# Kernel tuning notes

Measured on AMD Instinct MI355X. Metric: run time of the kernel, lower is better.

The kernel has to match this reference:

```python
import jax, jax.numpy as jnp
import numpy as np

B, L, DIM = 2, 2048, 1024
H, D = 16, 64  # n_heads, head_dim; H*D == DIM


def setup_inputs() -> dict:
    key = jax.random.key(0)
    ks = jax.random.split(key, 5)
    s = 0.02
    return {
        "x": jax.random.normal(ks[0], (B, L, DIM), dtype=jnp.float32),
        "Wq": jax.random.normal(ks[1], (DIM, H * D), dtype=jnp.float32) * s,
        "Wk": jax.random.normal(ks[2], (DIM, H * D), dtype=jnp.float32) * s,
        "Wv": jax.random.normal(ks[3], (DIM, H * D), dtype=jnp.float32) * s,
        "Wo": jax.random.normal(ks[4], (H * D, DIM), dtype=jnp.float32) * s,
    }


def reference(x, Wq, Wk, Wv, Wo):
    b, l, _ = x.shape
    scale = 1.0 / np.sqrt(D).astype(np.float32)
    # QKV projections -> [b, h, l, d]
    q = (x @ Wq).reshape(b, l, H, D).transpose(0, 2, 1, 3)
    k = (x @ Wk).reshape(b, l, H, D).transpose(0, 2, 1, 3)
    v = (x @ Wv).reshape(b, l, H, D).transpose(0, 2, 1, 3)
    # dense scores [b, h, l, l]
    scores = jnp.einsum("bhqd,bhkd->bhqk", q, k)
    # diagonal mask: each token cannot attend to itself
    diag = jnp.eye(l, dtype=bool)  # [l, l]
    scores = jnp.where(diag, -jnp.inf, scores)
    attn = jax.nn.softmax(scores * scale, axis=-1)
    out = jnp.einsum("bhqk,bhkd->bhqd", attn, v)
    out = out.transpose(0, 2, 1, 3).reshape(b, l, H * D)
    return out @ Wo
```

## Files before the change

kernel.cpp:

```cpp
#include <hip/hip_runtime.h>
#include <hip/hip_bf16.h>
#include <math.h>

#define L_SEQ 2048
#define DIMN  1024
#define NH    16
#define HD    64
#define NB    2
#define NTOK  (NB * L_SEQ)

typedef __attribute__((ext_vector_type(8))) short bf16x8;
typedef __attribute__((ext_vector_type(4))) float f32x4;
typedef __attribute__((ext_vector_type(16))) float f32x16;
typedef __attribute__((ext_vector_type(4))) short short4v;
typedef __attribute__((ext_vector_type(2))) unsigned uint32x2;

__device__ __forceinline__ short f2bf(float x) {
  return (short)__bfloat16_as_ushort(__float2bfloat16(x));
}
__device__ __forceinline__ float bf2f(short x) {
  union { unsigned u; float f; } c;
  c.u = ((unsigned)(unsigned short)x) << 16;
  return c.f;
}

__device__ __forceinline__ unsigned cvt_pk_bf16(float lo, float hi) {
  unsigned r;
  asm("v_cvt_pk_bf16_f32 %0, %1, %2" : "=v"(r) : "v"(lo), "v"(hi));
  return r;
}

__device__ __forceinline__ void permlane32_swap(unsigned& a, unsigned& b) {
  asm volatile("v_permlane32_swap_b32 %0, %1" : "+v"(a), "+v"(b));
}

__device__ __forceinline__ void gload_lds16(const short* gsrc, char* lds_dst) {
  __builtin_amdgcn_global_load_lds(
      (const __attribute__((address_space(1))) void*)gsrc,
      (__attribute__((address_space(3))) void*)lds_dst, 16, 0, 0);
}

__global__ __launch_bounds__(256) void cast_x_k(const float* __restrict__ in,
                                                short* __restrict__ out) {
  const int i = (blockIdx.x * 256 + threadIdx.x) * 8;
  float4 a = *(const float4*)(in + i);
  float4 b = *(const float4*)(in + i + 4);
  bf16x8 o;
  o[0] = f2bf(a.x); o[1] = f2bf(a.y); o[2] = f2bf(a.z); o[3] = f2bf(a.w);
  o[4] = f2bf(b.x); o[5] = f2bf(b.y); o[6] = f2bf(b.z); o[7] = f2bf(b.w);
  *(bf16x8*)(out + i) = o;
}

__global__ __launch_bounds__(256) void castT_k(const float* __restrict__ W,
                                               short* __restrict__ Wt) {
  __shared__ float s[64][65];
  const int tid = threadIdx.x;
  const int k0 = blockIdx.y * 64, n0 = blockIdx.x * 64;
#pragma unroll
  for (int i = 0; i < 4; ++i) {
    int idx = i * 256 + tid;
    int r = idx >> 4, c = (idx & 15) * 4;
    float4 v = *(const float4*)(W + (size_t)(k0 + r) * DIMN + n0 + c);
    s[r][c] = v.x; s[r][c + 1] = v.y; s[r][c + 2] = v.z; s[r][c + 3] = v.w;
  }
  __syncthreads();
#pragma unroll
  for (int i = 0; i < 4; ++i) {
    int idx = i * 256 + tid;
    int r = idx >> 4, c = (idx & 15) * 4;
    short4v o = { f2bf(s[c][r]), f2bf(s[c + 1][r]), f2bf(s[c + 2][r]), f2bf(s[c + 3][r]) };
    *(short4v*)(Wt + (size_t)(n0 + r) * DIMN + k0 + c) = o;
  }
}

__global__ __launch_bounds__(256) void vT_k(const short* __restrict__ V,
                                            short* __restrict__ Vt) {
  __shared__ short s[64][72];
  const int tid = threadIdx.x;
  const int bh = blockIdx.y;
  const int l0 = blockIdx.x * 64;
  const int row = tid >> 2, c0 = (tid & 3) * 16;
  const short* Vh = V + (size_t)bh * L_SEQ * HD;
  bf16x8 a = *(const bf16x8*)(Vh + (size_t)(l0 + row) * HD + c0);
  bf16x8 b = *(const bf16x8*)(Vh + (size_t)(l0 + row) * HD + c0 + 8);
#pragma unroll
  for (int j = 0; j < 8; ++j) { s[c0 + j][row] = a[j]; s[c0 + 8 + j][row] = b[j]; }
  __syncthreads();
  short* Vth = Vt + (size_t)bh * HD * L_SEQ;
  bf16x8 o0 = *(const bf16x8*)&s[row][c0];
  bf16x8 o1 = *(const bf16x8*)&s[row][c0 + 8];
  *(bf16x8*)(Vth + (size_t)row * L_SEQ + l0 + c0) = o0;
  *(bf16x8*)(Vth + (size_t)row * L_SEQ + l0 + c0 + 8) = o1;
}

template <int MODE>
__global__ __launch_bounds__(256) void mm_k(const short* __restrict__ A,
                                            const short* __restrict__ B0,
                                            const short* __restrict__ B1,
                                            const short* __restrict__ B2,
                                            void* __restrict__ C0,
                                            void* __restrict__ C1,
                                            void* __restrict__ C2,
                                            float scale0) {
  __shared__ char smem[65536];
  const int tid  = threadIdx.x;
  const int lane = tid & 63, wv = tid >> 6;
  const int g = lane >> 4, r16 = lane & 15;
  const int wr = wv >> 1, wc = wv & 1;
  const int row0 = blockIdx.y * 128, col0 = blockIdx.x * 128;
  const int z = blockIdx.z;
  const short* Bt = (z == 0) ? B0 : (z == 1 ? B1 : B2);
  const float scale = (MODE == 0 && z == 0) ? scale0 : 1.0f;

  f32x4 acc[4][4];
#pragma unroll
  for (int mi = 0; mi < 4; ++mi)
#pragma unroll
    for (int ni = 0; ni < 4; ++ni) acc[mi][ni] = (f32x4){0.f, 0.f, 0.f, 0.f};

  auto stage = [&](int buf, int kt) {
    const int k0 = kt * 64;
    char* As = smem + buf * 32768;
    char* Bs = As + 16384;
#pragma unroll
    for (int j = 0; j < 4; ++j) {
      const int o = j * 4096 + wv * 1024 + lane * 16;
      const int row = o >> 7;
      const int slot = (o >> 4) & 7;
      const int ksrc = k0 + ((slot ^ (row & 7)) << 3);
      gload_lds16(A  + (size_t)(row0 + row) * DIMN + ksrc, As + j * 4096 + wv * 1024);
      gload_lds16(Bt + (size_t)(col0 + row) * DIMN + ksrc, Bs + j * 4096 + wv * 1024);
    }
  };

  auto compute = [&](int buf) {
    const char* As = smem + buf * 32768;
    const char* Bs = As + 16384;
#pragma unroll
    for (int ks = 0; ks < 2; ++ks) {
      bf16x8 a[4], b[4];
#pragma unroll
      for (int mi = 0; mi < 4; ++mi) {
        const int row = wr * 64 + mi * 16 + r16;
        const int slot = (ks * 4 + g) ^ (row & 7);
        a[mi] = *(const bf16x8*)(As + row * 128 + slot * 16);
      }
#pragma unroll
      for (int ni = 0; ni < 4; ++ni) {
        const int row = wc * 64 + ni * 16 + r16;
        const int slot = (ks * 4 + g) ^ (row & 7);
        b[ni] = *(const bf16x8*)(Bs + row * 128 + slot * 16);
      }
#pragma unroll
      for (int mi = 0; mi < 4; ++mi)
#pragma unroll
        for (int ni = 0; ni < 4; ++ni)
          acc[mi][ni] = __builtin_amdgcn_mfma_f32_16x16x32_bf16(a[mi], b[ni], acc[mi][ni], 0, 0, 0);
    }
  };

  stage(0, 0);
  __syncthreads();
  int cur = 0;
  for (int kt = 0; kt < DIMN / 64 - 1; ++kt) {
    stage(cur ^ 1, kt + 1);
    compute(cur);
    __syncthreads();
    cur ^= 1;
  }
  compute(cur);

  void* Cp = (z == 0) ? C0 : (z == 1 ? C1 : C2);
#pragma unroll
  for (int mi = 0; mi < 4; ++mi) {
#pragma unroll
    for (int reg = 0; reg < 4; ++reg) {
      const int t = row0 + wr * 64 + mi * 16 + 4 * g + reg;
#pragma unroll
      for (int ni = 0; ni < 4; ++ni) {
        const int n = col0 + wc * 64 + ni * 16 + r16;
        if (MODE == 0) {
          const int b = t >> 11, l = t & (L_SEQ - 1);
          const int h = n >> 6, d = n & 63;
          ((short*)Cp)[(((size_t)(b * NH + h)) * L_SEQ + l) * HD + d] =
              f2bf(acc[mi][ni][reg] * scale);
        } else {
          ((float*)Cp)[(size_t)t * DIMN + n] = acc[mi][ni][reg];
        }
      }
    }
  }
}

__global__ __launch_bounds__(256) void attn_k(const short* __restrict__ Q,
                                              const short* __restrict__ K,
                                              const short* __restrict__ Vt,
                                              short* __restrict__ Op0,
                                              short* __restrict__ Op1,
                                              float* __restrict__ Lp) {
  __shared__ char kv[2][16384];

  const int tid  = threadIdx.x;
  const int wave = tid >> 6, lane = tid & 63;
  const int h = lane >> 5, r32 = lane & 31;

  const int id = blockIdx.x + 32 * blockIdx.y;
  const int j8 = id >> 3;
  const int bh = (id & 7) * 4 + (j8 >> 5);
  const int qtile = (j8 >> 1) & 15;
  const int split = j8 & 1;

  const int qbase = qtile * 128 + wave * 32;
  const int dtile = qtile * 2 + (wave >> 1);
  const int qg = qbase + r32;
  const int kbase = split * 16;

  const short* Qh  = Q  + (size_t)bh * L_SEQ * HD;
  const short* Kh  = K  + (size_t)bh * L_SEQ * HD;
  const short* Vth = Vt + (size_t)bh * HD * L_SEQ;

  bf16x8 qv[4];
#pragma unroll
  for (int ks = 0; ks < 4; ++ks)
    qv[ks] = *(const bf16x8*)(Qh + (size_t)qg * HD + ks * 16 + 8 * h);

  float lsum = 0.f;
  f32x16 o32[2];
#pragma unroll
  for (int db = 0; db < 2; ++db)
#pragma unroll
    for (int r = 0; r < 16; ++r) o32[db][r] = 0.f;

  const int sw = r32 & 7;
  const int rbase = r32 * 128;

  const int si1 = 256 + tid;
  const int row0s = tid >> 3,  c0s = (((tid & 7) ^ (row0s & 7)) << 3);
  const int row1s = si1 >> 3,  c1s = (((si1 & 7) ^ (row1s & 7)) << 3);
  const short* kp0 = Kh + (size_t)(split * 1024 + row0s) * HD + c0s;
  const short* kp1 = Kh + (size_t)(split * 1024 + row1s) * HD + c1s;
  const short* vp0 = Vth + (size_t)row0s * L_SEQ + split * 1024 + c0s;
  const short* vp1 = Vth + (size_t)row1s * L_SEQ + split * 1024 + c1s;
  const int ldo0 = tid * 16, ldo1 = si1 * 16;

  auto stage = [&](char* base) {
    gload_lds16(kp0, base + ldo0);
    gload_lds16(kp1, base + ldo1);
    gload_lds16(vp0, base + 8192 + ldo0);
    gload_lds16(vp1, base + 8192 + ldo1);
    kp0 += 64 * HD;
    kp1 += 64 * HD;
    vp0 += 64;
    vp1 += 64;
  };

  auto compute = [&](const char* Kb, int kt) {
    const char* Vb = Kb + 8192;

    f32x16 sa[2];
#pragma unroll
    for (int kb = 0; kb < 2; ++kb)
#pragma unroll
      for (int r = 0; r < 16; ++r) sa[kb][r] = 0.f;
    __builtin_amdgcn_s_setprio(1);
#pragma unroll
    for (int kb = 0; kb < 2; ++kb)
#pragma unroll
      for (int ks = 0; ks < 4; ++ks) {
        bf16x8 ak = *(const bf16x8*)(Kb + (kb * 32) * 128 + rbase + ((2 * ks + h) ^ sw) * 16);
        sa[kb] = __builtin_amdgcn_mfma_f32_32x32x16_bf16(ak, qv[ks], sa[kb], 0, 0, 0);
      }
    __builtin_amdgcn_s_setprio(0);

    if (kt == dtile) {
      const int tgt = qg - kt * 64;
#pragma unroll
      for (int kb = 0; kb < 2; ++kb)
#pragma unroll
        for (int r = 0; r < 16; ++r)
          if (kb * 32 + (r & 3) + 8 * (r >> 2) + 4 * h == tgt) sa[kb][r] = -INFINITY;
    }

#pragma unroll
    for (int kb = 0; kb < 2; ++kb)
#pragma unroll
      for (int r = 0; r < 16; ++r) sa[kb][r] = __builtin_amdgcn_exp2f(sa[kb][r]);
    float ps = 0.f;
#pragma unroll
    for (int kb = 0; kb < 2; ++kb) {
      float u0 = (sa[kb][0] + sa[kb][1]) + (sa[kb][2] + sa[kb][3]);
      float u1 = (sa[kb][4] + sa[kb][5]) + (sa[kb][6] + sa[kb][7]);
      float u2 = (sa[kb][8] + sa[kb][9]) + (sa[kb][10] + sa[kb][11]);
      float u3 = (sa[kb][12] + sa[kb][13]) + (sa[kb][14] + sa[kb][15]);
      ps += (u0 + u1) + (u2 + u3);
    }
    lsum += ps;

    bf16x8 bp[4];
#pragma unroll
    for (int kk = 0; kk < 4; ++kk) {
      const int kb = kk >> 1, s8 = (kk & 1) * 8;
      unsigned lo0 = cvt_pk_bf16(sa[kb][s8 + 0], sa[kb][s8 + 1]);
      unsigned lo1 = cvt_pk_bf16(sa[kb][s8 + 2], sa[kb][s8 + 3]);
      unsigned hi0 = cvt_pk_bf16(sa[kb][s8 + 4], sa[kb][s8 + 5]);
      unsigned hi1 = cvt_pk_bf16(sa[kb][s8 + 6], sa[kb][s8 + 7]);
      permlane32_swap(lo0, hi0);
      permlane32_swap(lo1, hi1);
      union { unsigned w[4]; bf16x8 v; } u;
      u.w[0] = lo0; u.w[1] = lo1; u.w[2] = hi0; u.w[3] = hi1;
      bp[kk] = u.v;
    }

    __builtin_amdgcn_s_setprio(1);
#pragma unroll
    for (int kk = 0; kk < 4; ++kk)
#pragma unroll
      for (int db = 0; db < 2; ++db) {
        bf16x8 av = *(const bf16x8*)(Vb + (db * 32) * 128 + rbase + ((2 * kk + h) ^ sw) * 16);
        o32[db] = __builtin_amdgcn_mfma_f32_32x32x16_bf16(av, bp[kk], o32[db], 0, 0, 0);
      }
    __builtin_amdgcn_s_setprio(0);
  };

#define STEP(CBUF, SBUF, KT, DO_STAGE)                        \
  do {                                                        \
    asm volatile("s_waitcnt vmcnt(0)" ::: "memory");          \
    __builtin_amdgcn_s_barrier();                             \
    __builtin_amdgcn_sched_barrier(0);                        \
    if (DO_STAGE) stage(SBUF);                                \
    compute(CBUF, KT);                                        \
  } while (0)

  stage(kv[0]);
  for (int i = 0; i < 14; i += 2) {
    STEP(kv[0], kv[1], kbase + i,     true);
    STEP(kv[1], kv[0], kbase + i + 1, true);
  }
  STEP(kv[0], kv[1], kbase + 14, true);
  STEP(kv[1], kv[0], kbase + 15, false);
#undef STEP

  lsum += __shfl_xor(lsum, 32);

  short* Opart = split ? Op1 : Op0;
  const size_t rowO = ((size_t)bh * L_SEQ + qg) * HD;
#pragma unroll
  for (int db = 0; db < 2; ++db)
#pragma unroll
    for (int grp = 0; grp < 4; ++grp) {
      const int d0 = db * 32 + grp * 8 + 4 * h;
      uint32x2 ow = { cvt_pk_bf16(o32[db][grp * 4 + 0], o32[db][grp * 4 + 1]),
                      cvt_pk_bf16(o32[db][grp * 4 + 2], o32[db][grp * 4 + 3]) };
      *(uint32x2*)(Opart + rowO + d0) = ow;
    }
  if (h == 0)
    Lp[(size_t)(split * NB * NH + bh) * L_SEQ + qg] = lsum;
}

__global__ __launch_bounds__(256) void combine_k(const short* __restrict__ Op0,
                                                 const short* __restrict__ Op1,
                                                 const float* __restrict__ Lp,
                                                 short* __restrict__ AO) {
  const int idx = blockIdx.x * 256 + threadIdx.x;
  const int d8 = (idx & 7) * 8;
  const int q  = (idx >> 3) & (L_SEQ - 1);
  const int bh = idx >> 14;
  const size_t po = ((size_t)bh * L_SEQ + q) * HD + d8;
  bf16x8 p0 = *(const bf16x8*)(Op0 + po);
  bf16x8 p1 = *(const bf16x8*)(Op1 + po);
  const float l0 = Lp[(size_t)bh * L_SEQ + q];
  const float l1 = Lp[(size_t)(NB * NH + bh) * L_SEQ + q];
  const float inv = 1.0f / (l0 + l1);
  const int b = bh >> 4, hh = bh & 15;
  bf16x8 o;
#pragma unroll
  for (int j = 0; j < 8; ++j)
    o[j] = f2bf((bf2f(p0[j]) + bf2f(p1[j])) * inv);
  *(bf16x8*)(AO + ((size_t)(b * L_SEQ + q)) * DIMN + hh * HD + d8) = o;
}

extern "C" void kernel_launch(void* const* d_in, const int* in_sizes, int n_in,
                              void* d_out, int out_size, void* d_ws, size_t ws_size,
                              hipStream_t stream) {
  const float* x  = (const float*)d_in[0];
  const float* Wq = (const float*)d_in[1];
  const float* Wk = (const float*)d_in[2];
  const float* Wv = (const float*)d_in[3];
  const float* Wo = (const float*)d_in[4];
  float* out = (float*)d_out;

  short* xb  = (short*)d_ws;
  short* Wqt = xb  + (size_t)NTOK * DIMN;
  short* Wkt = Wqt + (size_t)DIMN * DIMN;
  short* Wvt = Wkt + (size_t)DIMN * DIMN;
  short* Wot = Wvt + (size_t)DIMN * DIMN;
  short* Qb  = Wot + (size_t)DIMN * DIMN;
  short* Kb  = Qb  + (size_t)NTOK * DIMN;
  short* Vb  = Kb  + (size_t)NTOK * DIMN;
  short* Vtb = Vb  + (size_t)NTOK * DIMN;
  short* AO  = Vtb + (size_t)NTOK * DIMN;
  float* Lp  = (float*)(AO + (size_t)NTOK * DIMN);
  short* Op0 = xb;
  short* Op1 = Vb;

  cast_x_k<<<NTOK * DIMN / (256 * 8), 256, 0, stream>>>(x, xb);
  const dim3 tgrid(DIMN / 64, DIMN / 64);
  castT_k<<<tgrid, 256, 0, stream>>>(Wq, Wqt);
  castT_k<<<tgrid, 256, 0, stream>>>(Wk, Wkt);
  castT_k<<<tgrid, 256, 0, stream>>>(Wv, Wvt);
  castT_k<<<tgrid, 256, 0, stream>>>(Wo, Wot);

  mm_k<0><<<dim3(DIMN / 128, NTOK / 128, 3), 256, 0, stream>>>(
      xb, Wqt, Wkt, Wvt, Qb, Kb, Vb, 0.125f * 1.4426950408889634f);

  vT_k<<<dim3(L_SEQ / 64, NB * NH), 256, 0, stream>>>(Vb, Vtb);

  attn_k<<<dim3(32, NB * NH), 256, 0, stream>>>(Qb, Kb, Vtb, Op0, Op1, Lp);

  combine_k<<<2048, 256, 0, stream>>>(Op0, Op1, Lp, AO);

  mm_k<1><<<dim3(DIMN / 128, NTOK / 128, 1), 256, 0, stream>>>(
      AO, Wot, Wot, Wot, out, out, out, 1.0f);
}
```

Baseline: 131.8 us.

## Triple-buffer K/V tiles in attention and interleave score/softmax per block

Moves the attention kernel's K/V staging from double to triple buffering in shared memory (48KB per block), with a prefetch distance of two tiles and partial vmcnt waits, so global loads have more time to land before use. The score computation is also restructured per 32-key block so the exp and bf16 packing of one block can overlap the next block's MFMAs, which reduces live score registers. Launch bounds now request 3 blocks per CU. The extra LDS and the occupancy hint may constrain registers or occupancy.

```diff
diff --git a/kernel.cpp b/kernel.cpp
--- a/kernel.cpp
+++ b/kernel.cpp
@@ -192,13 +192,13 @@
   }
 }
 
-__global__ __launch_bounds__(256) void attn_k(const short* __restrict__ Q,
-                                              const short* __restrict__ K,
-                                              const short* __restrict__ Vt,
-                                              short* __restrict__ Op0,
-                                              short* __restrict__ Op1,
-                                              float* __restrict__ Lp) {
-  __shared__ char kv[2][16384];
+__global__ __launch_bounds__(256, 3) void attn_k(const short* __restrict__ Q,
+                                                 const short* __restrict__ K,
+                                                 const short* __restrict__ Vt,
+                                                 short* __restrict__ Op0,
+                                                 short* __restrict__ Op1,
+                                                 float* __restrict__ Lp) {
+  __shared__ char kv[3][16384];
 
   const int tid  = threadIdx.x;
   const int wave = tid >> 6, lane = tid & 63;
@@ -256,60 +256,52 @@
 
   auto compute = [&](const char* Kb, int kt) {
     const char* Vb = Kb + 8192;
-
-    f32x16 sa[2];
-#pragma unroll
-    for (int kb = 0; kb < 2; ++kb)
-#pragma unroll
-      for (int r = 0; r < 16; ++r) sa[kb][r] = 0.f;
-    __builtin_amdgcn_s_setprio(1);
-#pragma unroll
-    for (int kb = 0; kb < 2; ++kb)
+    bf16x8 bp[4];
+    float ps = 0.f;
+
+#pragma unroll
+    for (int kb = 0; kb < 2; ++kb) {
+      f32x16 sa;
+#pragma unroll
+      for (int r = 0; r < 16; ++r) sa[r] = 0.f;
+      __builtin_amdgcn_s_setprio(1);
 #pragma unroll
       for (int ks = 0; ks < 4; ++ks) {
         bf16x8 ak = *(const bf16x8*)(Kb + (kb * 32) * 128 + rbase + ((2 * ks + h) ^ sw) * 16);
-        sa[kb] = __builtin_amdgcn_mfma_f32_32x32x16_bf16(ak, qv[ks], sa[kb], 0, 0, 0);
-      }
-    __builtin_amdgcn_s_setprio(0);
-
-    if (kt == dtile) {
-      const int tgt = qg - kt * 64;
-#pragma unroll
-      for (int kb = 0; kb < 2; ++kb)
+        sa = __builtin_amdgcn_mfma_f32_32x32x16_bf16(ak, qv[ks], sa, 0, 0, 0);
+      }
+      __builtin_amdgcn_s_setprio(0);
+
+      if (kt == dtile) {
+        const int tgt = qg - kt * 64;
 #pragma unroll
         for (int r = 0; r < 16; ++r)
-          if (kb * 32 + (r & 3) + 8 * (r >> 2) + 4 * h == tgt) sa[kb][r] = -INFINITY;
-    }
-
-#pragma unroll
-    for (int kb = 0; kb < 2; ++kb)
-#pragma unroll
-      for (int r = 0; r < 16; ++r) sa[kb][r] = __builtin_amdgcn_exp2f(sa[kb][r]);
-    float ps = 0.f;
-#pragma unroll
-    for (int kb = 0; kb < 2; ++kb) {
-      float u0 = (sa[kb][0] + sa[kb][1]) + (sa[kb][2] + sa[kb][3]);
-      float u1 = (sa[kb][4] + sa[kb][5]) + (sa[kb][6] + sa[kb][7]);
-      float u2 = (sa[kb][8] + sa[kb][9]) + (sa[kb][10] + sa[kb][11]);
-      float u3 = (sa[kb][12] + sa[kb][13]) + (sa[kb][14] + sa[kb][15]);
+          if (kb * 32 + (r & 3) + 8 * (r >> 2) + 4 * h == tgt) sa[r] = -INFINITY;
+      }
+
+#pragma unroll
+      for (int r = 0; r < 16; ++r) sa[r] = __builtin_amdgcn_exp2f(sa[r]);
+      float u0 = (sa[0] + sa[1]) + (sa[2] + sa[3]);
+      float u1 = (sa[4] + sa[5]) + (sa[6] + sa[7]);
+      float u2 = (sa[8] + sa[9]) + (sa[10] + sa[11]);
+      float u3 = (sa[12] + sa[13]) + (sa[14] + sa[15]);
       ps += (u0 + u1) + (u2 + u3);
+
+#pragma unroll
+      for (int half = 0; half < 2; ++half) {
+        const int s8 = half * 8;
+        unsigned lo0 = cvt_pk_bf16(sa[s8 + 0], sa[s8 + 1]);
+        unsigned lo1 = cvt_pk_bf16(sa[s8 + 2], sa[s8 + 3]);
+        unsigned hi0 = cvt_pk_bf16(sa[s8 + 4], sa[s8 + 5]);
+        unsigned hi1 = cvt_pk_bf16(sa[s8 + 6], sa[s8 + 7]);
+        permlane32_swap(lo0, hi0);
+        permlane32_swap(lo1, hi1);
+        union { unsigned w[4]; bf16x8 v; } u;
+        u.w[0] = lo0; u.w[1] = lo1; u.w[2] = hi0; u.w[3] = hi1;
+        bp[kb * 2 + half] = u.v;
+      }
     }
     lsum += ps;
-
-    bf16x8 bp[4];
-#pragma unroll
-    for (int kk = 0; kk < 4; ++kk) {
-      const int kb = kk >> 1, s8 = (kk & 1) * 8;
-      unsigned lo0 = cvt_pk_bf16(sa[kb][s8 + 0], sa[kb][s8 + 1]);
-      unsigned lo1 = cvt_pk_bf16(sa[kb][s8 + 2], sa[kb][s8 + 3]);
-      unsigned hi0 = cvt_pk_bf16(sa[kb][s8 + 4], sa[kb][s8 + 5]);
-      unsigned hi1 = cvt_pk_bf16(sa[kb][s8 + 6], sa[kb][s8 + 7]);
-      permlane32_swap(lo0, hi0);
-      permlane32_swap(lo1, hi1);
-      union { unsigned w[4]; bf16x8 v; } u;
-      u.w[0] = lo0; u.w[1] = lo1; u.w[2] = hi0; u.w[3] = hi1;
-      bp[kk] = u.v;
-    }
 
     __builtin_amdgcn_s_setprio(1);
 #pragma unroll
@@ -322,23 +314,34 @@
     __builtin_amdgcn_s_setprio(0);
   };
 
-#define STEP(CBUF, SBUF, KT, DO_STAGE)                        \
+#define STEPC(CBUF, SBUF, KT)                                 \
   do {                                                        \
-    asm volatile("s_waitcnt vmcnt(0)" ::: "memory");          \
+    asm volatile("s_waitcnt vmcnt(4)" ::: "memory");          \
     __builtin_amdgcn_s_barrier();                             \
     __builtin_amdgcn_sched_barrier(0);                        \
-    if (DO_STAGE) stage(SBUF);                                \
+    stage(SBUF);                                              \
     compute(CBUF, KT);                                        \
   } while (0)
 
   stage(kv[0]);
-  for (int i = 0; i < 14; i += 2) {
-    STEP(kv[0], kv[1], kbase + i,     true);
-    STEP(kv[1], kv[0], kbase + i + 1, true);
+  stage(kv[1]);
+
+  for (int i = 0; i < 12; i += 3) {
+    STEPC(kv[0], kv[2], kbase + i);
+    STEPC(kv[1], kv[0], kbase + i + 1);
+    STEPC(kv[2], kv[1], kbase + i + 2);
   }
-  STEP(kv[0], kv[1], kbase + 14, true);
-  STEP(kv[1], kv[0], kbase + 15, false);
-#undef STEP
+  STEPC(kv[0], kv[2], kbase + 12);
+  STEPC(kv[1], kv[0], kbase + 13);
+  asm volatile("s_waitcnt vmcnt(4)" ::: "memory");
+  __builtin_amdgcn_s_barrier();
+  __builtin_amdgcn_sched_barrier(0);
+  compute(kv[2], kbase + 14);
+  asm volatile("s_waitcnt vmcnt(0)" ::: "memory");
+  __builtin_amdgcn_s_barrier();
+  __builtin_amdgcn_sched_barrier(0);
+  compute(kv[0], kbase + 15);
+#undef STEPC
 
   lsum += __shfl_xor(lsum, 32);
 
```

Measured after the change: 168.7 us. 28.0% more time.
